# Optimization experiments

Measured on AMD Instinct MI355X. Metric: run time of the kernel, lower is better.

Reference implementation:

```python
import jax, jax.numpy as jnp
import numpy as np

B, T, DIM = 2, 2048, 2048
N_HEAD, N_GROUP = 16, 4
KV_HEAD = N_HEAD // N_GROUP
HEAD_DIM = DIM // N_HEAD


def setup_inputs() -> dict:
    key = jax.random.key(0)
    ks = jax.random.split(key, 7)
    x = jax.random.normal(ks[0], (B, T, DIM), dtype=jnp.float32)
    # rotary tables: last dim = head_dim // 2 (interleaved real/imag pairs)
    pos = jnp.arange(T, dtype=jnp.float32)[:, None]
    inv_freq = 1.0 / (10000.0 ** (jnp.arange(0, HEAD_DIM, 2, dtype=jnp.float32) / HEAD_DIM))
    angles = pos * inv_freq[None, :]  # [T, HEAD_DIM//2]
    freqs_cos = jnp.cos(angles)
    freqs_sin = jnp.sin(angles)
    scale = 0.02
    wq = jax.random.normal(ks[1], (DIM, N_HEAD * HEAD_DIM), dtype=jnp.float32) * scale
    wk = jax.random.normal(ks[2], (DIM, KV_HEAD * HEAD_DIM), dtype=jnp.float32) * scale
    wv = jax.random.normal(ks[3], (DIM, KV_HEAD * HEAD_DIM), dtype=jnp.float32) * scale
    wo = jax.random.normal(ks[4], (N_HEAD * HEAD_DIM, DIM), dtype=jnp.float32) * scale
    return {"x": x, "freqs_cos": freqs_cos, "freqs_sin": freqs_sin,
            "wq": wq, "wk": wk, "wv": wv, "wo": wo}


def _apply_rope(t, cos, sin):
    # t: [B, T, H, D]; interleaved pairs (..., -1, 2) as in torch reference
    tr = t.reshape(*t.shape[:-1], -1, 2)
    r, i = tr[..., 0], tr[..., 1]
    c = cos[None, :, None, :]  # [1, T, 1, D//2]
    s = sin[None, :, None, :]
    out = jnp.stack([r * c - i * s, r * s + i * c], axis=-1)
    return out.reshape(t.shape)


def reference(x, freqs_cos, freqs_sin, wq, wk, wv, wo):
    Bx, Tx, C = x.shape
    xq = (x @ wq).reshape(Bx, Tx, N_HEAD, HEAD_DIM)
    xk = (x @ wk).reshape(Bx, Tx, KV_HEAD, HEAD_DIM)
    xv = (x @ wv).reshape(Bx, Tx, KV_HEAD, HEAD_DIM)
    xq = _apply_rope(xq, freqs_cos, freqs_sin)
    xk = _apply_rope(xk, freqs_cos, freqs_sin)
    # repeat_kv: each kv head repeated n_group times consecutively
    xk = jnp.repeat(xk, N_GROUP, axis=2)  # [B, T, N_HEAD, D]
    xv = jnp.repeat(xv, N_GROUP, axis=2)
    scale = HEAD_DIM ** -0.5
    att = jnp.einsum('bqhd,bkhd->bhqk', xq, xk) * scale
    causal = jnp.tril(jnp.ones((Tx, Tx), dtype=bool))
    att = jnp.where(causal[None, None], att, -jnp.inf)
    att = jax.nn.softmax(att, axis=-1)
    out = jnp.einsum('bhqk,bkhd->bqhd', att, xv).reshape(Bx, Tx, N_HEAD * HEAD_DIM)
    return out @ wo
```

## Files before the change

### kernel.cpp

```cpp
#include <hip/hip_runtime.h>

#define TB 2
#define TT 2048
#define TDIM 2048
#define NHEADS 16
#define KVHEADS 4
#define HD 128

typedef unsigned short u16;
typedef unsigned int u32;
typedef __attribute__((ext_vector_type(8))) short short8;
typedef __attribute__((ext_vector_type(4))) float float4_t;

__device__ __forceinline__ float b2f(u16 u) {
    union { u32 i; float f; } v; v.i = ((u32)u) << 16; return v.f;
}
__device__ __forceinline__ u16 f2b(float f) {
    union { float f; u32 i; } v; v.f = f;
    u32 r = (v.i + 0x7FFFu + ((v.i >> 16) & 1u)) >> 16;
    return (u16)r;
}
__device__ __forceinline__ u32 fbits(float f) {
    union { float f; u32 i; } v; v.f = f; return v.i;
}

__device__ __forceinline__ void gl_lds16(const void* g, void* l) {
    __builtin_amdgcn_global_load_lds((const __attribute__((address_space(1))) void*)g,
                                     (__attribute__((address_space(3))) void*)l, 16, 0, 0);
}

template <bool F32OUT, bool ROPE>
__global__ __launch_bounds__(256, 3)
void gemm_bt(const u16* __restrict__ A, const u16* __restrict__ BT,
             void* __restrict__ Cv, int M, int N, int K,
             const float* __restrict__ fc, const float* __restrict__ fs) {
    __shared__ __align__(16) u16 As[128 * 64];
    __shared__ __align__(16) u16 Bs[128 * 64];
    const int tid  = threadIdx.x;
    const int wave = tid >> 6, lane = tid & 63;
    const int quad = lane >> 4, l16 = lane & 15;
    const int wm = wave >> 1, wn = wave & 1;
    const int row0 = blockIdx.y * 128, col0 = blockIdx.x * 128;

    float4_t acc[4][4];
#pragma unroll
    for (int i = 0; i < 4; i++)
#pragma unroll
        for (int j = 0; j < 4; j++) acc[i][j] = (float4_t){0.f, 0.f, 0.f, 0.f};

    for (int kk = 0; kk < K; kk += 64) {
        __syncthreads();
#pragma unroll
        for (int i = 0; i < 4; i++) {
            int n = i * 256 + wave * 64 + lane;
            int r = n >> 3, c = (n & 7) ^ (r & 7);
            gl_lds16(A  + (size_t)(row0 + r) * K + kk + c * 8, &As[(i * 256 + wave * 64) * 8]);
            gl_lds16(BT + (size_t)(col0 + r) * K + kk + c * 8, &Bs[(i * 256 + wave * 64) * 8]);
        }
        __syncthreads();
#pragma unroll
        for (int ks = 0; ks < 2; ks++) {
            short8 af[4], bf[4];
#pragma unroll
            for (int mt = 0; mt < 4; mt++) {
                int m = wm * 64 + mt * 16 + l16;
                af[mt] = *(const short8*)&As[(m * 8 + ((ks * 4 + quad) ^ (l16 & 7))) * 8];
            }
#pragma unroll
            for (int nt = 0; nt < 4; nt++) {
                int n = wn * 64 + nt * 16 + l16;
                bf[nt] = *(const short8*)&Bs[(n * 8 + ((ks * 4 + quad) ^ (l16 & 7))) * 8];
            }
#pragma unroll
            for (int mt = 0; mt < 4; mt++)
#pragma unroll
                for (int nt = 0; nt < 4; nt++)
                    acc[mt][nt] = __builtin_amdgcn_mfma_f32_16x16x32_bf16(
                        af[mt], bf[nt], acc[mt][nt], 0, 0, 0);
        }
    }
    const bool do_rope = ROPE && (col0 < 2560);
#pragma unroll
    for (int mt = 0; mt < 4; mt++)
#pragma unroll
        for (int nt = 0; nt < 4; nt++)
#pragma unroll
            for (int r = 0; r < 4; r++) {
                int row = row0 + wm * 64 + mt * 16 + quad * 4 + r;
                int col = col0 + wn * 64 + nt * 16 + l16;
                float v = acc[mt][nt][r];
                if (ROPE && do_rope) {
                    float other = __shfl_xor(v, 1, 64);
                    int t = row & (TT - 1);
                    int i0 = (col & (HD - 1)) >> 1;
                    float c = fc[t * 64 + i0], s = fs[t * 64 + i0];
                    v = (col & 1) ? fmaf(v, c, other * s) : fmaf(v, c, -other * s);
                }
                if (F32OUT)
                    ((float*)Cv)[(size_t)row * N + col] = v;
                else
                    ((u16*)Cv)[(size_t)row * N + col] = f2b(v);
            }
}

__global__ void cvt_transpose4(const float* __restrict__ wq, const float* __restrict__ wk,
                               const float* __restrict__ wv, const float* __restrict__ wo,
                               u16* __restrict__ WT, u16* __restrict__ woT) {
    int bx = blockIdx.x;
    const float* in; u16* out; int cols, cx;
    if (bx < 64)      { in = wq; out = WT;                         cols = 2048; cx = bx; }
    else if (bx < 80) { in = wk; out = WT + (size_t)2048 * 2048;   cols = 512;  cx = bx - 64; }
    else if (bx < 96) { in = wv; out = WT + (size_t)2560 * 2048;   cols = 512;  cx = bx - 80; }
    else              { in = wo; out = woT;                        cols = 2048; cx = bx - 96; }
    const int rows = 2048;
    __shared__ u16 tile[32][33];
    int c0 = cx * 32, r0 = blockIdx.y * 32;
    int tx = threadIdx.x & 31, ty = threadIdx.x >> 5;
#pragma unroll
    for (int i = 0; i < 4; i++)
        tile[ty + i * 8][tx] = f2b(in[(size_t)(r0 + ty + i * 8) * cols + c0 + tx]);
    __syncthreads();
#pragma unroll
    for (int i = 0; i < 4; i++)
        out[(size_t)(c0 + ty + i * 8) * rows + r0 + tx] = tile[tx][ty + i * 8];
}

__global__ void cvt_bf16(const float* __restrict__ in, u16* __restrict__ out) {
    size_t i = ((size_t)blockIdx.x * 256 + threadIdx.x) * 4;
    float4 v = *(const float4*)(in + i);
    ushort4 o;
    o.x = f2b(v.x); o.y = f2b(v.y); o.z = f2b(v.z); o.w = f2b(v.w);
    *(ushort4*)(out + i) = o;
}

__global__ void transpose_v(const u16* __restrict__ QKV, u16* __restrict__ Vt) {
    int z = blockIdx.z, b = z >> 2, kv = z & 3;
    const u16* in = QKV + (size_t)b * TT * 3072 + 2560 + kv * HD;
    u16* out = Vt + (size_t)z * HD * TT;
    __shared__ u16 tile[32][33];
    int t0 = blockIdx.x * 32, d0 = blockIdx.y * 32;
    int tx = threadIdx.x & 31, ty = threadIdx.x >> 5;
#pragma unroll
    for (int i = 0; i < 4; i++)
        tile[ty + i * 8][tx] = in[(size_t)(t0 + ty + i * 8) * 3072 + d0 + tx];
    __syncthreads();
#pragma unroll
    for (int i = 0; i < 4; i++)
        out[(size_t)(d0 + ty + i * 8) * TT + t0 + tx] = tile[tx][ty + i * 8];
}

#define PSTR 72
__global__ __launch_bounds__(256, 2)
void attn(const u16* __restrict__ QKV, const u16* __restrict__ Vt,
          u16* __restrict__ O) {
    const int x  = blockIdx.x;
    const int y  = blockIdx.y;
    const int b  = y >> 3;
    const int hp = y & 7;
    const int kvh = hp >> 1;
    const int hb  = kvh * 4 + (hp & 1) * 2;
    const int qb  = b ? (31 - x) : x;
    const int tid = threadIdx.x, w = tid >> 6, lane = tid & 63;
    const int quad = lane >> 4, l16 = lane & 15;

    __shared__ __align__(16) u16 Ks[2][64 * 128];
    __shared__ __align__(16) u16 Vs[128 * 64];
    __shared__ __align__(16) u16 Ps[8][16 * PSTR];

    const u16* Kbase = QKV + (size_t)b * TT * 3072 + 2048 + kvh * HD;
    const u16* Vbase = Vt + (size_t)(b * 4 + kvh) * HD * TT;
    const float Cl = 0.12753102474f;

    auto stageK = [&](int kt, int bb) {
#pragma unroll
        for (int i = 0; i < 4; i++) {
            int n = i * 256 + w * 64 + lane;
            int r = n >> 4, c = (n & 15) ^ (r & 15);
            gl_lds16(Kbase + (size_t)(kt * 64 + r) * 3072 + c * 8,
                     &Ks[bb][(i * 256 + w * 64) * 8]);
        }
    };
    auto stageV = [&](int kt) {
#pragma unroll
        for (int i = 0; i < 4; i++) {
            int n = i * 256 + w * 64 + lane;
            int d = n >> 3, c = (n & 7) ^ (d & 7);
            gl_lds16(Vbase + (size_t)d * TT + kt * 64 + c * 8,
                     &Vs[(i * 256 + w * 64) * 8]);
        }
    };

    stageK(0, 0);

    short8 qf[2][4];
#pragma unroll
    for (int hd = 0; hd < 2; hd++) {
        const u16* Qrow = QKV + ((size_t)b * TT + qb * 64 + w * 16 + l16) * 3072
                          + (hb + hd) * HD;
#pragma unroll
        for (int ks = 0; ks < 4; ks++)
            qf[hd][ks] = *(const short8*)(Qrow + ks * 32 + quad * 8);
    }

    float4_t o[2][8];
#pragma unroll
    for (int hd = 0; hd < 2; hd++)
#pragma unroll
        for (int i = 0; i < 8; i++) o[hd][i] = (float4_t){0.f, 0.f, 0.f, 0.f};
    float mi[2] = {-1e30f, -1e30f}, li[2] = {0.f, 0.f};
    const int qg = qb * 64 + w * 16 + l16;

    for (int kt = 0; kt <= qb; kt++) {
        const int cur = kt & 1;
        __syncthreads();
        stageV(kt);

        float4_t st[2][4];
#pragma unroll
        for (int hd = 0; hd < 2; hd++)
#pragma unroll
            for (int nt = 0; nt < 4; nt++) st[hd][nt] = (float4_t){0.f, 0.f, 0.f, 0.f};
#pragma unroll
        for (int ks = 0; ks < 4; ks++) {
            short8 af[4];
#pragma unroll
            for (int nt = 0; nt < 4; nt++)
                af[nt] = *(const short8*)&Ks[cur][((nt * 16 + l16) * 16 +
                                                  ((ks * 4 + quad) ^ l16)) * 8];
#pragma unroll
            for (int nt = 0; nt < 4; nt++) {
                st[0][nt] = __builtin_amdgcn_mfma_f32_16x16x32_bf16(
                    af[nt], qf[0][ks], st[0][nt], 0, 0, 0);
                st[1][nt] = __builtin_amdgcn_mfma_f32_16x16x32_bf16(
                    af[nt], qf[1][ks], st[1][nt], 0, 0, 0);
            }
        }

        const bool diag = (kt == qb);
        float alpha[2];
#pragma unroll
        for (int hd = 0; hd < 2; hd++) {
            if (diag) {
#pragma unroll
                for (int nt = 0; nt < 4; nt++)
#pragma unroll
                    for (int r = 0; r < 4; r++) {
                        int key = kt * 64 + nt * 16 + quad * 4 + r;
                        if (key > qg) st[hd][nt][r] = -3e38f;
                    }
            }
            float pm = -3e38f;
#pragma unroll
            for (int nt = 0; nt < 4; nt++)
#pragma unroll
                for (int r = 0; r < 4; r++) pm = fmaxf(pm, st[hd][nt][r]);
            pm = fmaxf(pm, __shfl_xor(pm, 16, 64));
            pm = fmaxf(pm, __shfl_xor(pm, 32, 64));
            float mnew = fmaxf(mi[hd], pm);
            alpha[hd] = __builtin_amdgcn_exp2f((mi[hd] - mnew) * Cl);
            mi[hd] = mnew;
            const float mC = mnew * Cl;
            float rs = 0.f;
#pragma unroll
            for (int nt = 0; nt < 4; nt++)
#pragma unroll
                for (int r = 0; r < 4; r++) {
                    float e = __builtin_amdgcn_exp2f(fmaf(st[hd][nt][r], Cl, -mC));
                    st[hd][nt][r] = e;
                    rs += e;
                }
            rs += __shfl_xor(rs, 16, 64);
            rs += __shfl_xor(rs, 32, 64);
            li[hd] = li[hd] * alpha[hd] + rs;

#pragma unroll
            for (int nt = 0; nt < 4; nt++) {
                uint2 pk;
                pk.x = __builtin_amdgcn_perm(fbits(st[hd][nt][1]), fbits(st[hd][nt][0]), 0x07060302u);
                pk.y = __builtin_amdgcn_perm(fbits(st[hd][nt][3]), fbits(st[hd][nt][2]), 0x07060302u);
                *(uint2*)&Ps[w * 2 + hd][l16 * PSTR + nt * 16 + quad * 4] = pk;
            }
            float a_o[4];
#pragma unroll
            for (int r = 0; r < 4; r++) a_o[r] = __shfl(alpha[hd], quad * 4 + r, 64);
#pragma unroll
            for (int n2 = 0; n2 < 8; n2++)
#pragma unroll
                for (int r = 0; r < 4; r++) o[hd][n2][r] *= a_o[r];
        }

        __syncthreads();
        if (kt < qb) stageK(kt + 1, cur ^ 1);

#pragma unroll
        for (int ks2 = 0; ks2 < 2; ks2++) {
            short8 apA = *(const short8*)&Ps[w * 2 + 0][l16 * PSTR + ks2 * 32 + quad * 8];
            short8 apB = *(const short8*)&Ps[w * 2 + 1][l16 * PSTR + ks2 * 32 + quad * 8];
#pragma unroll
            for (int n2 = 0; n2 < 8; n2++) {
                short8 bv = *(const short8*)&Vs[((n2 * 16 + l16) * 8 +
                                                ((ks2 * 4 + quad) ^ (l16 & 7))) * 8];
                o[0][n2] = __builtin_amdgcn_mfma_f32_16x16x32_bf16(apA, bv, o[0][n2], 0, 0, 0);
                o[1][n2] = __builtin_amdgcn_mfma_f32_16x16x32_bf16(apB, bv, o[1][n2], 0, 0, 0);
            }
        }
    }

#pragma unroll
    for (int hd = 0; hd < 2; hd++) {
        float l_o[4];
#pragma unroll
        for (int r = 0; r < 4; r++) l_o[r] = __shfl(li[hd], quad * 4 + r, 64);
        u16* Ob2 = O + ((size_t)b * TT + qb * 64 + w * 16) * TDIM + (hb + hd) * HD;
#pragma unroll
        for (int n2 = 0; n2 < 8; n2++)
#pragma unroll
            for (int r = 0; r < 4; r++)
                Ob2[(size_t)(quad * 4 + r) * TDIM + n2 * 16 + l16] =
                    f2b(o[hd][n2][r] / l_o[r]);
    }
}

extern "C" void kernel_launch(void* const* d_in, const int* in_sizes, int n_in,
                              void* d_out, int out_size, void* d_ws, size_t ws_size,
                              hipStream_t stream) {
    const float* x  = (const float*)d_in[0];
    const float* fc = (const float*)d_in[1];
    const float* fs = (const float*)d_in[2];
    const float* wq = (const float*)d_in[3];
    const float* wk = (const float*)d_in[4];
    const float* wv = (const float*)d_in[5];
    const float* wo = (const float*)d_in[6];
    float* out = (float*)d_out;

    char* ws = (char*)d_ws;
    size_t off = 0;
    auto alloc = [&](size_t bytes) -> void* {
        void* p = ws + off;
        off += (bytes + 255) & ~(size_t)255;
        return p;
    };
    u16* xb  = (u16*)alloc((size_t)4096 * 2048 * 2);
    u16* WT  = (u16*)alloc((size_t)3072 * 2048 * 2);
    u16* woT = (u16*)alloc((size_t)2048 * 2048 * 2);
    u16* QKV = (u16*)alloc((size_t)4096 * 3072 * 2);
    u16* Vtb = (u16*)alloc((size_t)4096 * 512 * 2);
    u16* Ob  = (u16*)alloc((size_t)4096 * 2048 * 2);

    dim3 blk(256);
    cvt_bf16<<<dim3(8192), blk, 0, stream>>>(x, xb);
    cvt_transpose4<<<dim3(160, 64), blk, 0, stream>>>(wq, wk, wv, wo, WT, woT);
    gemm_bt<false, true><<<dim3(24, 32), blk, 0, stream>>>(
        xb, WT, QKV, 4096, 3072, 2048, fc, fs);
    transpose_v<<<dim3(64, 4, 8), blk, 0, stream>>>(QKV, Vtb);
    attn<<<dim3(32, 16), blk, 0, stream>>>(QKV, Vtb, Ob);
    gemm_bt<true, false><<<dim3(16, 32), blk, 0, stream>>>(
        Ob, woT, out, 4096, 2048, 2048, nullptr, nullptr);
}
```

Before: 288.7 us.

## Fuse prep kernels, add MFMA priority hints, lazy softmax rescale, reciprocal normalize

Merges the x bf16 conversion and the weight transpose-convert into one launch, which removes a kernel launch and its tail. In the attention loop it raises wave priority around the MFMA blocks with s_setprio. It also skips the online-softmax max update and the rescale of the output accumulator when no lane's row max grew by more than a threshold. It replaces the per-element division in the epilogue with a multiply by a precomputed reciprocal. The lazy rescale relies on the exp2 values staying bounded under the stale max, which keeps the result exact but adds a wave-wide vote per tile.

New measurement: 311.5 us. 1.08x slower.

```diff
diff --git a/kernel.cpp b/kernel.cpp
--- a/kernel.cpp
+++ b/kernel.cpp
@@ -103,10 +103,22 @@
             }
 }
 
-__global__ void cvt_transpose4(const float* __restrict__ wq, const float* __restrict__ wk,
-                               const float* __restrict__ wv, const float* __restrict__ wo,
-                               u16* __restrict__ WT, u16* __restrict__ woT) {
-    int bx = blockIdx.x;
+__global__ void prep(const float* __restrict__ x, u16* __restrict__ xb,
+                     const float* __restrict__ wq, const float* __restrict__ wk,
+                     const float* __restrict__ wv, const float* __restrict__ wo,
+                     u16* __restrict__ WT, u16* __restrict__ woT) {
+    const int bid = blockIdx.x;
+    if (bid < 8192) {
+        size_t i = ((size_t)bid * 256 + threadIdx.x) * 4;
+        float4 v = *(const float4*)(x + i);
+        ushort4 o;
+        o.x = f2b(v.x); o.y = f2b(v.y); o.z = f2b(v.z); o.w = f2b(v.w);
+        *(ushort4*)(xb + i) = o;
+        return;
+    }
+    const int rem = bid - 8192;
+    const int bx = rem % 160;
+    const int by = rem / 160;
     const float* in; u16* out; int cols, cx;
     if (bx < 64)      { in = wq; out = WT;                         cols = 2048; cx = bx; }
     else if (bx < 80) { in = wk; out = WT + (size_t)2048 * 2048;   cols = 512;  cx = bx - 64; }
@@ -114,7 +126,7 @@
     else              { in = wo; out = woT;                        cols = 2048; cx = bx - 96; }
     const int rows = 2048;
     __shared__ u16 tile[32][33];
-    int c0 = cx * 32, r0 = blockIdx.y * 32;
+    int c0 = cx * 32, r0 = by * 32;
     int tx = threadIdx.x & 31, ty = threadIdx.x >> 5;
 #pragma unroll
     for (int i = 0; i < 4; i++)
@@ -123,14 +135,6 @@
 #pragma unroll
     for (int i = 0; i < 4; i++)
         out[(size_t)(c0 + ty + i * 8) * rows + r0 + tx] = tile[tx][ty + i * 8];
-}
-
-__global__ void cvt_bf16(const float* __restrict__ in, u16* __restrict__ out) {
-    size_t i = ((size_t)blockIdx.x * 256 + threadIdx.x) * 4;
-    float4 v = *(const float4*)(in + i);
-    ushort4 o;
-    o.x = f2b(v.x); o.y = f2b(v.y); o.z = f2b(v.z); o.w = f2b(v.w);
-    *(ushort4*)(out + i) = o;
 }
 
 __global__ void transpose_v(const u16* __restrict__ QKV, u16* __restrict__ Vt) {
@@ -227,6 +231,7 @@
             for (int nt = 0; nt < 4; nt++)
                 af[nt] = *(const short8*)&Ks[cur][((nt * 16 + l16) * 16 +
                                                   ((ks * 4 + quad) ^ l16)) * 8];
+            __builtin_amdgcn_s_setprio(1);
 #pragma unroll
             for (int nt = 0; nt < 4; nt++) {
                 st[0][nt] = __builtin_amdgcn_mfma_f32_16x16x32_bf16(
@@ -234,10 +239,10 @@
                 st[1][nt] = __builtin_amdgcn_mfma_f32_16x16x32_bf16(
                     af[nt], qf[1][ks], st[1][nt], 0, 0, 0);
             }
+            __builtin_amdgcn_s_setprio(0);
         }
 
         const bool diag = (kt == qb);
-        float alpha[2];
 #pragma unroll
         for (int hd = 0; hd < 2; hd++) {
             if (diag) {
@@ -256,10 +261,14 @@
                 for (int r = 0; r < 4; r++) pm = fmaxf(pm, st[hd][nt][r]);
             pm = fmaxf(pm, __shfl_xor(pm, 16, 64));
             pm = fmaxf(pm, __shfl_xor(pm, 32, 64));
-            float mnew = fmaxf(mi[hd], pm);
-            alpha[hd] = __builtin_amdgcn_exp2f((mi[hd] - mnew) * Cl);
-            mi[hd] = mnew;
-            const float mC = mnew * Cl;
+            const bool need = !__all(pm - mi[hd] <= 62.7f);
+            float alpha_v = 1.f;
+            if (need) {
+                float mnew = fmaxf(mi[hd], pm);
+                alpha_v = __builtin_amdgcn_exp2f((mi[hd] - mnew) * Cl);
+                mi[hd] = mnew;
+            }
+            const float mC = mi[hd] * Cl;
             float rs = 0.f;
 #pragma unroll
             for (int nt = 0; nt < 4; nt++)
@@ -271,7 +280,7 @@
                 }
             rs += __shfl_xor(rs, 16, 64);
             rs += __shfl_xor(rs, 32, 64);
-            li[hd] = li[hd] * alpha[hd] + rs;
+            li[hd] = li[hd] * alpha_v + rs;
 
 #pragma unroll
             for (int nt = 0; nt < 4; nt++) {
@@ -280,13 +289,15 @@
                 pk.y = __builtin_amdgcn_perm(fbits(st[hd][nt][3]), fbits(st[hd][nt][2]), 0x07060302u);
                 *(uint2*)&Ps[w * 2 + hd][l16 * PSTR + nt * 16 + quad * 4] = pk;
             }
-            float a_o[4];
-#pragma unroll
-            for (int r = 0; r < 4; r++) a_o[r] = __shfl(alpha[hd], quad * 4 + r, 64);
-#pragma unroll
-            for (int n2 = 0; n2 < 8; n2++)
-#pragma unroll
-                for (int r = 0; r < 4; r++) o[hd][n2][r] *= a_o[r];
+            if (need) {
+                float a_o[4];
+#pragma unroll
+                for (int r = 0; r < 4; r++) a_o[r] = __shfl(alpha_v, quad * 4 + r, 64);
+#pragma unroll
+                for (int n2 = 0; n2 < 8; n2++)
+#pragma unroll
+                    for (int r = 0; r < 4; r++) o[hd][n2][r] *= a_o[r];
+            }
         }
 
         __syncthreads();
@@ -296,6 +307,7 @@
         for (int ks2 = 0; ks2 < 2; ks2++) {
             short8 apA = *(const short8*)&Ps[w * 2 + 0][l16 * PSTR + ks2 * 32 + quad * 8];
             short8 apB = *(const short8*)&Ps[w * 2 + 1][l16 * PSTR + ks2 * 32 + quad * 8];
+            __builtin_amdgcn_s_setprio(1);
 #pragma unroll
             for (int n2 = 0; n2 < 8; n2++) {
                 short8 bv = *(const short8*)&Vs[((n2 * 16 + l16) * 8 +
@@ -303,21 +315,22 @@
                 o[0][n2] = __builtin_amdgcn_mfma_f32_16x16x32_bf16(apA, bv, o[0][n2], 0, 0, 0);
                 o[1][n2] = __builtin_amdgcn_mfma_f32_16x16x32_bf16(apB, bv, o[1][n2], 0, 0, 0);
             }
+            __builtin_amdgcn_s_setprio(0);
         }
     }
 
 #pragma unroll
     for (int hd = 0; hd < 2; hd++) {
-        float l_o[4];
-#pragma unroll
-        for (int r = 0; r < 4; r++) l_o[r] = __shfl(li[hd], quad * 4 + r, 64);
+        float linv[4];
+#pragma unroll
+        for (int r = 0; r < 4; r++) linv[r] = 1.0f / __shfl(li[hd], quad * 4 + r, 64);
         u16* Ob2 = O + ((size_t)b * TT + qb * 64 + w * 16) * TDIM + (hb + hd) * HD;
 #pragma unroll
         for (int n2 = 0; n2 < 8; n2++)
 #pragma unroll
             for (int r = 0; r < 4; r++)
                 Ob2[(size_t)(quad * 4 + r) * TDIM + n2 * 16 + l16] =
-                    f2b(o[hd][n2][r] / l_o[r]);
+                    f2b(o[hd][n2][r] * linv[r]);
     }
 }
 
@@ -348,8 +361,7 @@
     u16* Ob  = (u16*)alloc((size_t)4096 * 2048 * 2);
 
     dim3 blk(256);
-    cvt_bf16<<<dim3(8192), blk, 0, stream>>>(x, xb);
-    cvt_transpose4<<<dim3(160, 64), blk, 0, stream>>>(wq, wk, wv, wo, WT, woT);
+    prep<<<dim3(8192 + 160 * 64), blk, 0, stream>>>(x, xb, wq, wk, wv, wo, WT, woT);
     gemm_bt<false, true><<<dim3(24, 32), blk, 0, stream>>>(
         xb, WT, QKV, 4096, 3072, 2048, fc, fs);
     transpose_v<<<dim3(64, 4, 8), blk, 0, stream>>>(QKV, Vtb);
```
